# Optimization experiments

Hardware: AMD Instinct MI355X
Metric: run time of the kernel (lower is better)

Reference implementation:

```python
import jax, jax.numpy as jnp
import numpy as np

H = 16          # num_heads
HD = 64         # head_dim = latent_dim // num_heads
RHD = 32        # rope_head_dim = head_dim // 2
NHD = 32        # nope_head_dim
Q_LAT = 256     # latent_dim // compression_ratio
KV_LAT = 204    # xf_latent_dim // (compression_ratio + 1)
MAX_LEN = 2048
THETA = 10000.0
EPS = 1e-5


def _rope_tables():
    half = RHD // 2  # 16
    freqs = 1.0 / THETA ** (np.arange(half, dtype=np.float32) / half)
    t = np.arange(MAX_LEN, dtype=np.float32)
    ang = np.outer(t, freqs)  # (MAX_LEN, half)
    return jnp.asarray(np.cos(ang)), jnp.asarray(np.sin(ang))

COS, SIN = _rope_tables()


def _ln(x, g, b):
    m = jnp.mean(x, axis=-1, keepdims=True)
    v = jnp.var(x, axis=-1, keepdims=True)
    return (x - m) * jax.lax.rsqrt(v + EPS) * g + b


def _rope(t, cos, sin):
    # t: (..., L, RHD); cos/sin: (L, RHD//2); interleaved even/odd convention
    ev, od = t[..., 0::2], t[..., 1::2]
    oe = ev * cos - od * sin
    oo = ev * sin + od * cos
    return jnp.stack([oe, oo], axis=-1).reshape(t.shape)


def setup_inputs() -> dict:
    key = jax.random.key(0)
    ks = jax.random.split(key, 12)
    D = 1024
    s = 0.02
    return {
        "x": jax.random.normal(ks[0], (2, 2048, D), jnp.float32),
        "xf": jax.random.normal(ks[1], (2, 2048, D), jnp.float32),
        "Wqc": jax.random.normal(ks[2], (D, Q_LAT), jnp.float32) * s,
        "gq": jnp.ones((Q_LAT,), jnp.float32),
        "bq": jnp.zeros((Q_LAT,), jnp.float32),
        "Wq_rope": jax.random.normal(ks[3], (Q_LAT, H * RHD), jnp.float32) * s,
        "Wq_nope": jax.random.normal(ks[4], (Q_LAT, H * NHD), jnp.float32) * s,
        "Wkvc": jax.random.normal(ks[5], (D, KV_LAT), jnp.float32) * s,
        "gkv": jnp.ones((KV_LAT,), jnp.float32),
        "bkv": jnp.zeros((KV_LAT,), jnp.float32),
        "Wk_nope": jax.random.normal(ks[6], (KV_LAT, H * NHD), jnp.float32) * s,
        "Wv": jax.random.normal(ks[7], (KV_LAT, H * HD), jnp.float32) * s,
        "Wkr": jax.random.normal(ks[8], (D, RHD), jnp.float32) * s,
        "Wo": jax.random.normal(ks[9], (D, D), jnp.float32) * s,
        "bo": jnp.zeros((D,), jnp.float32),
    }


def reference(x, xf, Wqc, gq, bq, Wq_rope, Wq_nope, Wkvc, gkv, bkv, Wk_nope, Wv, Wkr, Wo, bo):
    B, T, D = x.shape
    S = xf.shape[1]

    # query path: compress -> LN -> decoupled decompress
    ql = _ln(x @ Wqc, gq, bq)                                   # (B,T,Q_LAT)
    q_nope = (ql @ Wq_nope).reshape(B, T, H, NHD).transpose(0, 2, 1, 3)  # (B,H,T,NHD)
    q_rope = (ql @ Wq_rope).reshape(B, T, H, RHD).transpose(0, 2, 1, 3)  # (B,H,T,RHD)

    # key/value path: compress -> LN -> decompress; shared single rope head
    kvl = _ln(xf @ Wkvc, gkv, bkv)                              # (B,S,KV_LAT)
    k_nope = (kvl @ Wk_nope).reshape(B, S, H, NHD).transpose(0, 2, 1, 3)  # (B,H,S,NHD)
    v = (kvl @ Wv).reshape(B, S, H, HD).transpose(0, 2, 1, 3)   # (B,H,S,HD)
    k_rope = (xf @ Wkr).reshape(B, S, 1, RHD).transpose(0, 2, 1, 3)       # (B,1,S,RHD)

    q_rope = _rope(q_rope, COS[:T], SIN[:T])
    k_rope = _rope(k_rope, COS[:S], SIN[:S]) / H
    k_rope = jnp.broadcast_to(k_rope, (B, H, S, RHD))

    q = jnp.concatenate([q_nope, q_rope], axis=-1)              # (B,H,T,HD)
    k = jnp.concatenate([k_nope, k_rope], axis=-1)              # (B,H,S,HD)

    scale = 1.0 / jnp.sqrt(jnp.asarray(HD, q.dtype))
    scores = jnp.einsum("bhtd,bhsd->bhts", q, k) * scale
    attn = jax.nn.softmax(scores, axis=-1)
    o = jnp.einsum("bhts,bhsd->bhtd", attn, v)                  # (B,H,T,HD)
    o = o.transpose(0, 2, 1, 3).reshape(B, T, H * HD)
    return o @ Wo + bo
```

## Files before the change

### kernel.cpp

```cpp
#include <hip/hip_runtime.h>
#include <hip/hip_bf16.h>
#include <math.h>

#define SEQ 2048

typedef __bf16 bf16x8 __attribute__((ext_vector_type(8)));
typedef float  f32x4  __attribute__((ext_vector_type(4)));

__device__ __forceinline__ unsigned short f2bf(float f) {
  __bf16 h = (__bf16)f;
  return __builtin_bit_cast(unsigned short, h);
}

__device__ __forceinline__ void gload16(const unsigned short* g, unsigned short* l) {
  __builtin_amdgcn_global_load_lds(
      (const __attribute__((address_space(1))) void*)g,
      (__attribute__((address_space(3))) void*)l, 16, 0, 0);
}

#define CLOG (0.125f * 1.44269504f)

struct WPrep {
  const float* src[8];
  unsigned short* dst[8];
  int K[8], N[8], NR[8], KC[8], nb[8];
  float2* cst;
};

__global__ __launch_bounds__(256) void wprep_kernel(WPrep p)
{
  __shared__ float tile[32][33];
  int bid = blockIdx.x;
  if (bid < 128) {
    const int idx = bid * 256 + threadIdx.x;
    const int pos = idx >> 4, i = idx & 15;
    const float freq = exp2f(-(float)i * 0.8304820237f);
    const float ang = (float)pos * freq;
    p.cst[idx] = make_float2(cosf(ang), sinf(ang));
    return;
  }
  bid -= 128;
  int di = 0;
  while (bid >= p.nb[di]) { bid -= p.nb[di]; ++di; }
  const float* src = p.src[di];
  unsigned short* dst = p.dst[di];
  const int K = p.K[di], N = p.N[di], KC = p.KC[di];
  const int nkx = KC >> 5;
  const int k0 = (bid % nkx) * 32, n0 = (bid / nkx) * 32;
  const int tx = threadIdx.x & 31, ty = threadIdx.x >> 5;
  for (int r = ty; r < 32; r += 8) {
    const int k = k0 + r, n = n0 + tx;
    tile[r][tx] = (k < K && n < N) ? src[(long)k * N + n] : 0.0f;
  }
  __syncthreads();
  for (int r = ty; r < 32; r += 8) {
    const int n = n0 + r, k = k0 + tx;
    dst[(long)n * KC + k] = f2bf(tile[tx][r]);
  }
}

template <int EPI, bool AF32>
__device__ __forceinline__ void gemm_body(
    unsigned short* smem,
    const void* __restrict__ Av, const unsigned short* __restrict__ BT,
    const float* __restrict__ bias, const float2* __restrict__ cst,
    void* __restrict__ C0v, void* __restrict__ C1v, int K, int N,
    int bx, int by)
{
  unsigned short* As = smem;
  unsigned short* Bs = smem + 2 * 128 * 32;
  const int tid = threadIdx.x;
  const int w = tid >> 6, lane = tid & 63;
  const int ln16 = lane & 15, quad = lane >> 4;
  const int wm = (w >> 1) * 64, wn = (w & 1) * 64;
  const int m0 = by * 128, n0 = bx * 128;
  const int rr = tid >> 2, cc = (tid & 3) * 8;

  const unsigned short* A = (const unsigned short*)Av;
  const float* Af = (const float*)Av;

  auto stageB = [&](int ib, int k0) {
    gload16(&BT[(long)(n0 + rr)      * K + k0 + cc], &Bs[ib * 4096 + rr * 32 + cc]);
    gload16(&BT[(long)(n0 + 64 + rr) * K + k0 + cc], &Bs[ib * 4096 + (64 + rr) * 32 + cc]);
  };
  auto stageAbf = [&](int ib, int k0) {
    gload16(&A[(long)(m0 + rr)      * K + k0 + cc], &As[ib * 4096 + rr * 32 + cc]);
    gload16(&A[(long)(m0 + 64 + rr) * K + k0 + cc], &As[ib * 4096 + (64 + rr) * 32 + cc]);
  };
  auto writeAf32 = [&](int ib, const float4& a0, const float4& a1,
                       const float4& a2, const float4& a3) {
    ushort4 u;
    u.x = f2bf(a0.x); u.y = f2bf(a0.y); u.z = f2bf(a0.z); u.w = f2bf(a0.w);
    *(ushort4*)&As[ib * 4096 + rr * 32 + cc] = u;
    u.x = f2bf(a1.x); u.y = f2bf(a1.y); u.z = f2bf(a1.z); u.w = f2bf(a1.w);
    *(ushort4*)&As[ib * 4096 + rr * 32 + cc + 4] = u;
    u.x = f2bf(a2.x); u.y = f2bf(a2.y); u.z = f2bf(a2.z); u.w = f2bf(a2.w);
    *(ushort4*)&As[ib * 4096 + (64 + rr) * 32 + cc] = u;
    u.x = f2bf(a3.x); u.y = f2bf(a3.y); u.z = f2bf(a3.z); u.w = f2bf(a3.w);
    *(ushort4*)&As[ib * 4096 + (64 + rr) * 32 + cc + 4] = u;
  };

  f32x4 acc[4][4];
#pragma unroll
  for (int i = 0; i < 4; ++i)
#pragma unroll
    for (int j = 0; j < 4; ++j)
#pragma unroll
      for (int r = 0; r < 4; ++r) acc[i][j][r] = 0.0f;

  stageB(0, 0);
  if (AF32) {
    float4 a0 = *(const float4*)&Af[(long)(m0 + rr)      * K + cc];
    float4 a1 = *(const float4*)&Af[(long)(m0 + rr)      * K + cc + 4];
    float4 a2 = *(const float4*)&Af[(long)(m0 + 64 + rr) * K + cc];
    float4 a3 = *(const float4*)&Af[(long)(m0 + 64 + rr) * K + cc + 4];
    writeAf32(0, a0, a1, a2, a3);
  } else {
    stageAbf(0, 0);
  }

  int ib = 0;
  for (int k0 = 0; k0 < K; k0 += 32, ib ^= 1) {
    __syncthreads();
    const int kn = k0 + 32;
    float4 a0, a1, a2, a3;
    if (kn < K) {
      stageB(ib ^ 1, kn);
      if (AF32) {
        a0 = *(const float4*)&Af[(long)(m0 + rr)      * K + kn + cc];
        a1 = *(const float4*)&Af[(long)(m0 + rr)      * K + kn + cc + 4];
        a2 = *(const float4*)&Af[(long)(m0 + 64 + rr) * K + kn + cc];
        a3 = *(const float4*)&Af[(long)(m0 + 64 + rr) * K + kn + cc + 4];
      } else {
        stageAbf(ib ^ 1, kn);
      }
    }
    bf16x8 fa[4], fb[4];
#pragma unroll
    for (int i = 0; i < 4; ++i) fa[i] = *(const bf16x8*)&As[ib * 4096 + (wm + i * 16 + ln16) * 32 + quad * 8];
#pragma unroll
    for (int j = 0; j < 4; ++j) fb[j] = *(const bf16x8*)&Bs[ib * 4096 + (wn + j * 16 + ln16) * 32 + quad * 8];
#pragma unroll
    for (int i = 0; i < 4; ++i)
#pragma unroll
      for (int j = 0; j < 4; ++j)
        acc[i][j] = __builtin_amdgcn_mfma_f32_16x16x32_bf16(fa[i], fb[j], acc[i][j], 0, 0, 0);
    if (AF32 && kn < K) writeAf32(ib ^ 1, a0, a1, a2, a3);
  }

#pragma unroll
  for (int i = 0; i < 4; ++i) {
    const int row0 = m0 + wm + i * 16 + quad * 4;
#pragma unroll
    for (int j = 0; j < 4; ++j) {
      const int col = n0 + wn + j * 16 + ln16;
      if (EPI == 0 || EPI == 1) {
        float* C = (float*)C0v;
        float bv = (EPI == 1) ? bias[col] : 0.0f;
#pragma unroll
        for (int r = 0; r < 4; ++r) C[(long)(row0 + r) * N + col] = acc[i][j][r] + bv;
      } else if (EPI == 3) {
        if (n0 < 512) {
          unsigned short* qn = (unsigned short*)C0v;
#pragma unroll
          for (int r = 0; r < 4; ++r) qn[(long)(row0 + r) * 512 + col] = f2bf(acc[i][j][r] * CLOG);
        } else {
          unsigned short* qr = (unsigned short*)C1v;
          const int c = col - 512;
          const int d = c & 31;
#pragma unroll
          for (int r = 0; r < 4; ++r) {
            const float v = acc[i][j][r];
            const float p = __shfl_xor(v, 1);
            const float2 t = cst[((row0 + r) & (SEQ - 1)) * 16 + (d >> 1)];
            const float o = ((d & 1) == 0) ? (v * t.x - p * t.y) : (p * t.y + v * t.x);
            qr[(long)(row0 + r) * 512 + c] = f2bf(o * CLOG);
          }
        }
      } else if (EPI == 4) {
        if (n0 < 256) {
          float* kvl = (float*)C0v;
#pragma unroll
          for (int r = 0; r < 4; ++r) kvl[(long)(row0 + r) * 256 + col] = acc[i][j][r];
        } else if (wn == 0 && j < 2) {
          unsigned short* kr = (unsigned short*)C1v;
          const int d = col - 256;
#pragma unroll
          for (int r = 0; r < 4; ++r) {
            const float v = acc[i][j][r];
            const float p = __shfl_xor(v, 1);
            const float2 t = cst[((row0 + r) & (SEQ - 1)) * 16 + (d >> 1)];
            const float o = ((d & 1) == 0) ? (v * t.x - p * t.y) : (p * t.y + v * t.x);
            kr[(long)(row0 + r) * 32 + d] = f2bf(o * 0.0625f);
          }
        }
      } else if (EPI == 5) {
        if (n0 < 512) {
          unsigned short* kn = (unsigned short*)C0v;
#pragma unroll
          for (int r = 0; r < 4; ++r) kn[(long)(row0 + r) * 512 + col] = f2bf(acc[i][j][r]);
        } else {
          unsigned short* vv = (unsigned short*)C1v;
          const int c = col - 512;
#pragma unroll
          for (int r = 0; r < 4; ++r) vv[(long)(row0 + r) * 1024 + c] = f2bf(acc[i][j][r]);
        }
      }
    }
  }
}

template <int EPI, bool AF32>
__global__ __launch_bounds__(256) void gemm_mfma(
    const void* __restrict__ Av, const unsigned short* __restrict__ BT,
    const float* __restrict__ bias, const float2* __restrict__ cst,
    void* __restrict__ C0v, void* __restrict__ C1v, int K, int N)
{
  __shared__ unsigned short smem[4 * 128 * 32];
  gemm_body<EPI, AF32>(smem, Av, BT, bias, cst, C0v, C1v, K, N, blockIdx.x, blockIdx.y);
}

template <int E0, bool AF0, int E1, bool AF1>
__global__ __launch_bounds__(256) void gemm_dual(
    const void* __restrict__ A0, const unsigned short* __restrict__ BT0,
    void* __restrict__ C00, void* __restrict__ C01, int K0, int N0, int nx0,
    const void* __restrict__ A1, const unsigned short* __restrict__ BT1,
    void* __restrict__ C10, void* __restrict__ C11, int K1, int N1,
    const float2* __restrict__ cst)
{
  __shared__ unsigned short smem[4 * 128 * 32];
  if (blockIdx.z == 0) {
    if ((int)blockIdx.x >= nx0) return;
    gemm_body<E0, AF0>(smem, A0, BT0, nullptr, cst, C00, C01, K0, N0, blockIdx.x, blockIdx.y);
  } else {
    gemm_body<E1, AF1>(smem, A1, BT1, nullptr, cst, C10, C11, K1, N1, blockIdx.x, blockIdx.y);
  }
}

__global__ __launch_bounds__(256) void ln2_kernel(
    const float* __restrict__ Xq, const float* __restrict__ Xkv,
    const float* __restrict__ gq, const float* __restrict__ bq,
    const float* __restrict__ gkv, const float* __restrict__ bkv,
    unsigned short* __restrict__ Yq, unsigned short* __restrict__ Ykv)
{
  const int row0 = blockIdx.x, tid = threadIdx.x;
  const bool isq = row0 < 4096;
  const int row = isq ? row0 : row0 - 4096;
  const float* X = isq ? Xq : Xkv;
  const float* g = isq ? gq : gkv;
  const float* b = isq ? bq : bkv;
  unsigned short* Y = isq ? Yq : Ykv;
  const int C = isq ? 256 : 204;
  const int Cp = isq ? 256 : 224;
  float v = (tid < C) ? X[(long)row * 256 + tid] : 0.0f;
  float s1 = v, s2 = v * v;
#pragma unroll
  for (int off = 1; off < 64; off <<= 1) {
    s1 += __shfl_xor(s1, off);
    s2 += __shfl_xor(s2, off);
  }
  __shared__ float rA[4], rB[4];
  const int wid = tid >> 6;
  if ((tid & 63) == 0) { rA[wid] = s1; rB[wid] = s2; }
  __syncthreads();
  s1 = rA[0] + rA[1] + rA[2] + rA[3];
  s2 = rB[0] + rB[1] + rB[2] + rB[3];
  const float mean = s1 / C;
  const float var  = s2 / C - mean * mean;
  const float r = rsqrtf(var + 1e-5f);
  if (tid < C) Y[(long)row * Cp + tid] = f2bf((v - mean) * r * g[tid] + b[tid]);
  else if (tid < Cp) Y[(long)row * Cp + tid] = 0;
}

__global__ __launch_bounds__(256) void transpose_v_kernel(
    const unsigned short* __restrict__ vf, unsigned short* __restrict__ vT)
{
  __shared__ unsigned short tile[64][72];
  const int bh = blockIdx.y;
  const int b = bh >> 4, h = bh & 15;
  const int s0 = blockIdx.x * 64;
  const int tid = threadIdx.x;
  for (int idx = tid; idx < 4096; idx += 256) {
    const int r = idx >> 6, c = idx & 63;
    tile[r][c] = vf[((long)b * SEQ + s0 + r) * 1024 + h * 64 + c];
  }
  __syncthreads();
  for (int idx = tid; idx < 4096; idx += 256) {
    const int d = idx >> 6, si = idx & 63;
    vT[((long)bh * 64 + d) * SEQ + s0 + si] = tile[si][d];
  }
}

#define KSTR 36
#define VSTR 68
#define PSTR 68
__global__ __launch_bounds__(256, 3) void attn_mfma_kernel(
    const unsigned short* __restrict__ qn, const unsigned short* __restrict__ qr,
    const unsigned short* __restrict__ kn, const unsigned short* __restrict__ kr,
    const unsigned short* __restrict__ vT, unsigned short* __restrict__ ob)
{
  __shared__ unsigned short Kn[2][64 * KSTR], Kr[2][64 * KSTR];
  __shared__ unsigned short Vs[2][64 * VSTR];
  __shared__ unsigned short Ps[128 * PSTR];
  const int bh = blockIdx.y;
  const int b = bh >> 4, h = bh & 15;
  const int t0 = blockIdx.x * 128;
  const int tid = threadIdx.x;
  const int w = tid >> 6, lane = tid & 63;
  const int ln16 = lane & 15, quad = lane >> 4;
  const int wrow = w * 32;
  const long bT = (long)b * SEQ;

  const int krow = tid >> 2, kc8 = (tid & 3) * 8;
  const int vd0 = tid >> 3, vc0 = (tid & 7) * 8;
  const int vd1 = (tid + 256) >> 3, vc1 = vc0;

  bf16x8 q0[2], q1[2];
#pragma unroll
  for (int g = 0; g < 2; ++g) {
    q0[g] = *(const bf16x8*)&qn[(bT + t0 + wrow + g * 16 + ln16) * 512 + h * 32 + quad * 8];
    q1[g] = *(const bf16x8*)&qr[(bT + t0 + wrow + g * 16 + ln16) * 512 + h * 32 + quad * 8];
  }

  auto loadKV = [&](int s0, bf16x8& rk0, bf16x8& rk1, bf16x8& rv0, bf16x8& rv1) {
    rk0 = *(const bf16x8*)&kn[(bT + s0 + krow) * 512 + h * 32 + kc8];
    rk1 = *(const bf16x8*)&kr[(bT + s0 + krow) * 32 + kc8];
    rv0 = *(const bf16x8*)&vT[((long)bh * 64 + vd0) * SEQ + s0 + vc0];
    rv1 = *(const bf16x8*)&vT[((long)bh * 64 + vd1) * SEQ + s0 + vc1];
  };
  auto writeKV = [&](int ib, bf16x8 rk0, bf16x8 rk1, bf16x8 rv0, bf16x8 rv1) {
    *(bf16x8*)&Kn[ib][krow * KSTR + kc8] = rk0;
    *(bf16x8*)&Kr[ib][krow * KSTR + kc8] = rk1;
    *(bf16x8*)&Vs[ib][vd0 * VSTR + vc0] = rv0;
    *(bf16x8*)&Vs[ib][vd1 * VSTR + vc1] = rv1;
  };

  bf16x8 ck0, ck1, cv0, cv1;
  bf16x8 nk0, nk1, nv0, nv1;
  loadKV(0, ck0, ck1, cv0, cv1);
  writeKV(0, ck0, ck1, cv0, cv1);
  loadKV(64, nk0, nk1, nv0, nv1);

  f32x4 o_acc[2][4];
#pragma unroll
  for (int g = 0; g < 2; ++g)
#pragma unroll
    for (int nt = 0; nt < 4; ++nt)
#pragma unroll
      for (int r = 0; r < 4; ++r) o_acc[g][nt][r] = 0.0f;
  float l_i[2] = {0.0f, 0.0f};

  int ib = 0;
  for (int s0 = 0; s0 < SEQ; s0 += 64, ib ^= 1) {
    __syncthreads();
    if (s0 + 64 < SEQ) {
      writeKV(ib ^ 1, nk0, nk1, nv0, nv1);
      if (s0 + 128 < SEQ) loadKV(s0 + 128, nk0, nk1, nv0, nv1);
    }

    bf16x8 kn_f[4], kr_f[4];
#pragma unroll
    for (int nt = 0; nt < 4; ++nt) {
      kn_f[nt] = *(const bf16x8*)&Kn[ib][(nt * 16 + ln16) * KSTR + quad * 8];
      kr_f[nt] = *(const bf16x8*)&Kr[ib][(nt * 16 + ln16) * KSTR + quad * 8];
    }

    f32x4 sf[2][4];
#pragma unroll
    for (int g = 0; g < 2; ++g) {
#pragma unroll
      for (int nt = 0; nt < 4; ++nt)
#pragma unroll
        for (int r = 0; r < 4; ++r) sf[g][nt][r] = 0.0f;
#pragma unroll
      for (int nt = 0; nt < 4; ++nt) {
        sf[g][nt] = __builtin_amdgcn_mfma_f32_16x16x32_bf16(kn_f[nt], q0[g], sf[g][nt], 0, 0, 0);
        sf[g][nt] = __builtin_amdgcn_mfma_f32_16x16x32_bf16(kr_f[nt], q1[g], sf[g][nt], 0, 0, 0);
      }
    }

#pragma unroll
    for (int g = 0; g < 2; ++g) {
      float rs = 0.0f;
      float pv[4][4];
#pragma unroll
      for (int nt = 0; nt < 4; ++nt)
#pragma unroll
        for (int r = 0; r < 4; ++r) {
          const float p = exp2f(sf[g][nt][r]);
          pv[nt][r] = p;
          rs += p;
        }
      rs += __shfl_xor(rs, 16);
      rs += __shfl_xor(rs, 32);
      l_i[g] += rs;
#pragma unroll
      for (int nt = 0; nt < 4; ++nt) {
        ushort4 u;
        u.x = f2bf(pv[nt][0]); u.y = f2bf(pv[nt][1]);
        u.z = f2bf(pv[nt][2]); u.w = f2bf(pv[nt][3]);
        *(ushort4*)&Ps[(wrow + g * 16 + ln16) * PSTR + nt * 16 + quad * 4] = u;
      }
    }

    bf16x8 v_f[2][4];
#pragma unroll
    for (int kk2 = 0; kk2 < 2; ++kk2)
#pragma unroll
      for (int nt = 0; nt < 4; ++nt)
        v_f[kk2][nt] = *(const bf16x8*)&Vs[ib][(nt * 16 + ln16) * VSTR + kk2 * 32 + quad * 8];

#pragma unroll
    for (int g = 0; g < 2; ++g) {
      bf16x8 a0 = *(const bf16x8*)&Ps[(wrow + g * 16 + ln16) * PSTR + quad * 8];
      bf16x8 a1 = *(const bf16x8*)&Ps[(wrow + g * 16 + ln16) * PSTR + 32 + quad * 8];
#pragma unroll
      for (int nt = 0; nt < 4; ++nt) {
        o_acc[g][nt] = __builtin_amdgcn_mfma_f32_16x16x32_bf16(a0, v_f[0][nt], o_acc[g][nt], 0, 0, 0);
        o_acc[g][nt] = __builtin_amdgcn_mfma_f32_16x16x32_bf16(a1, v_f[1][nt], o_acc[g][nt], 0, 0, 0);
      }
    }
  }

#pragma unroll
  for (int g = 0; g < 2; ++g) {
    const float lr = 1.0f / l_i[g];
    float lq[4];
#pragma unroll
    for (int r = 0; r < 4; ++r) lq[r] = __shfl(lr, quad * 4 + r);
#pragma unroll
    for (int r = 0; r < 4; ++r) {
      const long t = t0 + wrow + g * 16 + quad * 4 + r;
      const long base = (bT + t) * 1024 + h * 64 + ln16;
#pragma unroll
      for (int nt = 0; nt < 4; ++nt)
        ob[base + nt * 16] = f2bf(o_acc[g][nt][r] * lq[r]);
    }
  }
}

extern "C" void kernel_launch(void* const* d_in, const int* in_sizes, int n_in,
                              void* d_out, int out_size, void* d_ws, size_t ws_size,
                              hipStream_t stream) {
  const float* x       = (const float*)d_in[0];
  const float* xf      = (const float*)d_in[1];
  const float* Wqc     = (const float*)d_in[2];
  const float* gq      = (const float*)d_in[3];
  const float* bq      = (const float*)d_in[4];
  const float* Wq_rope = (const float*)d_in[5];
  const float* Wq_nope = (const float*)d_in[6];
  const float* Wkvc    = (const float*)d_in[7];
  const float* gkv     = (const float*)d_in[8];
  const float* bkv     = (const float*)d_in[9];
  const float* Wk_nope = (const float*)d_in[10];
  const float* Wv      = (const float*)d_in[11];
  const float* Wkr     = (const float*)d_in[12];
  const float* Wo      = (const float*)d_in[13];
  const float* bo      = (const float*)d_in[14];
  float* out = (float*)d_out;

  const long R = 4096;
  float* ws = (float*)d_ws;
  float* ql_f  = ws;
  float* kvl_f = ql_f + R * 256;
  float2* cst  = (float2*)(kvl_f + R * 256);
  unsigned short* us = (unsigned short*)(cst + 2048 * 16);
  unsigned short* ql_bf  = us;  us += R * 256;
  unsigned short* kvl_bf = us;  us += R * 224;
  unsigned short* qn_bf  = us;  us += R * 512;
  unsigned short* qr_bf  = us;  us += R * 512;
  unsigned short* kn_bf  = us;  us += R * 512;
  unsigned short* kr_bf  = us;  us += R * 32;
  unsigned short* v_bf   = us;  us += R * 1024;
  unsigned short* vT_bf  = us;  us += R * 1024;
  unsigned short* o_bf   = us;  us += R * 1024;
  unsigned short* WqcT   = us;  us += 256 * 1024;
  unsigned short* WkvkrT = us;  us += 384 * 1024;
  unsigned short* WqnqrT = us;  us += 1024 * 256;
  unsigned short* WknvT  = us;  us += 1536 * 224;
  unsigned short* WoT    = us;  us += 1024 * 1024;

  WPrep p;
  const float* srcs[8] = {Wqc, Wkvc, Wkr, Wq_nope, Wq_rope, Wk_nope, Wv, Wo};
  unsigned short* dsts[8] = {WqcT, WkvkrT, WkvkrT + 256 * 1024,
                             WqnqrT, WqnqrT + 512 * 256,
                             WknvT, WknvT + 512 * 224, WoT};
  const int Ks[8]  = {1024, 1024, 1024, 256, 256, 204, 204, 1024};
  const int Ns[8]  = {256, 204, 32, 512, 512, 512, 1024, 1024};
  const int NRs[8] = {256, 256, 128, 512, 512, 512, 1024, 1024};
  const int KCs[8] = {1024, 1024, 1024, 256, 256, 224, 224, 1024};
  int total = 128;
  for (int i = 0; i < 8; ++i) {
    p.src[i] = srcs[i]; p.dst[i] = dsts[i];
    p.K[i] = Ks[i]; p.N[i] = Ns[i]; p.NR[i] = NRs[i]; p.KC[i] = KCs[i];
    p.nb[i] = (KCs[i] / 32) * (NRs[i] / 32);
    total += p.nb[i];
  }
  p.cst = cst;
  wprep_kernel<<<total, 256, 0, stream>>>(p);

  gemm_dual<0, true, 4, true><<<dim3(3, 32, 2), 256, 0, stream>>>(
      x, WqcT, ql_f, nullptr, 1024, 256, 2,
      xf, WkvkrT, kvl_f, kr_bf, 1024, 384, cst);
  ln2_kernel<<<8192, 256, 0, stream>>>(ql_f, kvl_f, gq, bq, gkv, bkv, ql_bf, kvl_bf);
  gemm_dual<3, false, 5, false><<<dim3(12, 32, 2), 256, 0, stream>>>(
      ql_bf, WqnqrT, qn_bf, qr_bf, 256, 1024, 8,
      kvl_bf, WknvT, kn_bf, v_bf, 224, 1536, cst);
  transpose_v_kernel<<<dim3(32, 32), 256, 0, stream>>>(v_bf, vT_bf);
  attn_mfma_kernel<<<dim3(16, 32), 256, 0, stream>>>(qn_bf, qr_bf, kn_bf, kr_bf, vT_bf, o_bf);
  gemm_mfma<1, false><<<dim3(8, 32), 256, 0, stream>>>(o_bf, WoT, bo, nullptr, out, nullptr, 1024, 1024);
}
```

Measured before the change: 253.9 us.

## Fuse V transpose into GEMM epilogue and retile attention to 64-row blocks

The K/V decompression GEMM now stages its V output tile in shared memory and writes it directly in transposed (b,h,d,s) layout. This removes the separate transpose kernel and the intermediate v buffer. The attention kernel changes from 128 to 64 query rows per block (16 per wave), which doubles the grid to 1024 blocks and halves the P scratch. Block IDs are also remapped so each XCD handles a few heads, for L2 locality of K/V. The trade-off is that each K/V tile is now loaded twice as often, and the GEMM kernels need a larger shared-memory allocation.

```diff
diff --git a/kernel.cpp b/kernel.cpp
--- a/kernel.cpp
+++ b/kernel.cpp
@@ -148,6 +148,32 @@
     if (AF32 && kn < K) writeAf32(ib ^ 1, a0, a1, a2, a3);
   }
 
+  if (EPI == 5 && n0 >= 512) {
+    __syncthreads();
+#pragma unroll
+    for (int i = 0; i < 4; ++i) {
+      const int rl = wm + i * 16 + quad * 4;
+#pragma unroll
+      for (int j = 0; j < 4; ++j) {
+        const int cl = wn + j * 16 + ln16;
+        ushort4 u;
+        u.x = f2bf(acc[i][j][0]); u.y = f2bf(acc[i][j][1]);
+        u.z = f2bf(acc[i][j][2]); u.w = f2bf(acc[i][j][3]);
+        *(ushort4*)&smem[cl * 132 + rl] = u;
+      }
+    }
+    __syncthreads();
+    unsigned short* vT = (unsigned short*)C1v;
+    const int b = m0 >> 11, sbase = m0 & (SEQ - 1);
+    for (int q = tid; q < 128 * 16; q += 256) {
+      const int cl = q >> 4, sch = (q & 15) * 8;
+      bf16x8 val = *(const bf16x8*)&smem[cl * 132 + sch];
+      const int c = (n0 - 512) + cl;
+      const int hh = c >> 6, dd = c & 63;
+      *(bf16x8*)&vT[((long)(b * 16 + hh) * 64 + dd) * SEQ + sbase + sch] = val;
+    }
+    return;
+  }
 #pragma unroll
   for (int i = 0; i < 4; ++i) {
     const int row0 = m0 + wm + i * 16 + quad * 4;
@@ -195,16 +221,9 @@
           }
         }
       } else if (EPI == 5) {
-        if (n0 < 512) {
-          unsigned short* kn = (unsigned short*)C0v;
-#pragma unroll
-          for (int r = 0; r < 4; ++r) kn[(long)(row0 + r) * 512 + col] = f2bf(acc[i][j][r]);
-        } else {
-          unsigned short* vv = (unsigned short*)C1v;
-          const int c = col - 512;
-#pragma unroll
-          for (int r = 0; r < 4; ++r) vv[(long)(row0 + r) * 1024 + c] = f2bf(acc[i][j][r]);
-        }
+        unsigned short* kn = (unsigned short*)C0v;
+#pragma unroll
+        for (int r = 0; r < 4; ++r) kn[(long)(row0 + r) * 512 + col] = f2bf(acc[i][j][r]);
       }
     }
   }
@@ -216,7 +235,7 @@
     const float* __restrict__ bias, const float2* __restrict__ cst,
     void* __restrict__ C0v, void* __restrict__ C1v, int K, int N)
 {
-  __shared__ unsigned short smem[4 * 128 * 32];
+  __shared__ unsigned short smem[16896];
   gemm_body<EPI, AF32>(smem, Av, BT, bias, cst, C0v, C1v, K, N, blockIdx.x, blockIdx.y);
 }
 
@@ -228,7 +247,7 @@
     void* __restrict__ C10, void* __restrict__ C11, int K1, int N1,
     const float2* __restrict__ cst)
 {
-  __shared__ unsigned short smem[4 * 128 * 32];
+  __shared__ unsigned short smem[16896];
   if (blockIdx.z == 0) {
     if ((int)blockIdx.x >= nx0) return;
     gemm_body<E0, AF0>(smem, A0, BT0, nullptr, cst, C00, C01, K0, N0, blockIdx.x, blockIdx.y);
@@ -272,25 +291,6 @@
   else if (tid < Cp) Y[(long)row * Cp + tid] = 0;
 }
 
-__global__ __launch_bounds__(256) void transpose_v_kernel(
-    const unsigned short* __restrict__ vf, unsigned short* __restrict__ vT)
-{
-  __shared__ unsigned short tile[64][72];
-  const int bh = blockIdx.y;
-  const int b = bh >> 4, h = bh & 15;
-  const int s0 = blockIdx.x * 64;
-  const int tid = threadIdx.x;
-  for (int idx = tid; idx < 4096; idx += 256) {
-    const int r = idx >> 6, c = idx & 63;
-    tile[r][c] = vf[((long)b * SEQ + s0 + r) * 1024 + h * 64 + c];
-  }
-  __syncthreads();
-  for (int idx = tid; idx < 4096; idx += 256) {
-    const int d = idx >> 6, si = idx & 63;
-    vT[((long)bh * 64 + d) * SEQ + s0 + si] = tile[si][d];
-  }
-}
-
 #define KSTR 36
 #define VSTR 68
 #define PSTR 68
@@ -301,38 +301,37 @@
 {
   __shared__ unsigned short Kn[2][64 * KSTR], Kr[2][64 * KSTR];
   __shared__ unsigned short Vs[2][64 * VSTR];
-  __shared__ unsigned short Ps[128 * PSTR];
-  const int bh = blockIdx.y;
+  __shared__ unsigned short Ps[64 * PSTR];
+  const int id = blockIdx.x;
+  const int xcd = id & 7, j = id >> 3;
+  const int bh = xcd * 4 + (j & 3);
+  const int tile = j >> 2;
   const int b = bh >> 4, h = bh & 15;
-  const int t0 = blockIdx.x * 128;
+  const int t0 = tile * 64;
   const int tid = threadIdx.x;
   const int w = tid >> 6, lane = tid & 63;
   const int ln16 = lane & 15, quad = lane >> 4;
-  const int wrow = w * 32;
+  const int trow = w * 16;
   const long bT = (long)b * SEQ;
 
   const int krow = tid >> 2, kc8 = (tid & 3) * 8;
   const int vd0 = tid >> 3, vc0 = (tid & 7) * 8;
-  const int vd1 = (tid + 256) >> 3, vc1 = vc0;
-
-  bf16x8 q0[2], q1[2];
-#pragma unroll
-  for (int g = 0; g < 2; ++g) {
-    q0[g] = *(const bf16x8*)&qn[(bT + t0 + wrow + g * 16 + ln16) * 512 + h * 32 + quad * 8];
-    q1[g] = *(const bf16x8*)&qr[(bT + t0 + wrow + g * 16 + ln16) * 512 + h * 32 + quad * 8];
-  }
+  const int vd1 = vd0 + 32;
+
+  bf16x8 q0 = *(const bf16x8*)&qn[(bT + t0 + trow + ln16) * 512 + h * 32 + quad * 8];
+  bf16x8 q1 = *(const bf16x8*)&qr[(bT + t0 + trow + ln16) * 512 + h * 32 + quad * 8];
 
   auto loadKV = [&](int s0, bf16x8& rk0, bf16x8& rk1, bf16x8& rv0, bf16x8& rv1) {
     rk0 = *(const bf16x8*)&kn[(bT + s0 + krow) * 512 + h * 32 + kc8];
     rk1 = *(const bf16x8*)&kr[(bT + s0 + krow) * 32 + kc8];
     rv0 = *(const bf16x8*)&vT[((long)bh * 64 + vd0) * SEQ + s0 + vc0];
-    rv1 = *(const bf16x8*)&vT[((long)bh * 64 + vd1) * SEQ + s0 + vc1];
+    rv1 = *(const bf16x8*)&vT[((long)bh * 64 + vd1) * SEQ + s0 + vc0];
   };
   auto writeKV = [&](int ib, bf16x8 rk0, bf16x8 rk1, bf16x8 rv0, bf16x8 rv1) {
     *(bf16x8*)&Kn[ib][krow * KSTR + kc8] = rk0;
     *(bf16x8*)&Kr[ib][krow * KSTR + kc8] = rk1;
     *(bf16x8*)&Vs[ib][vd0 * VSTR + vc0] = rv0;
-    *(bf16x8*)&Vs[ib][vd1 * VSTR + vc1] = rv1;
+    *(bf16x8*)&Vs[ib][vd1 * VSTR + vc0] = rv1;
   };
 
   bf16x8 ck0, ck1, cv0, cv1;
@@ -341,14 +340,12 @@
   writeKV(0, ck0, ck1, cv0, cv1);
   loadKV(64, nk0, nk1, nv0, nv1);
 
-  f32x4 o_acc[2][4];
-#pragma unroll
-  for (int g = 0; g < 2; ++g)
-#pragma unroll
-    for (int nt = 0; nt < 4; ++nt)
-#pragma unroll
-      for (int r = 0; r < 4; ++r) o_acc[g][nt][r] = 0.0f;
-  float l_i[2] = {0.0f, 0.0f};
+  f32x4 o_acc[4];
+#pragma unroll
+  for (int nt = 0; nt < 4; ++nt)
+#pragma unroll
+    for (int r = 0; r < 4; ++r) o_acc[nt][r] = 0.0f;
+  float l_i = 0.0f;
 
   int ib = 0;
   for (int s0 = 0; s0 < SEQ; s0 += 64, ib ^= 1) {
@@ -358,84 +355,62 @@
       if (s0 + 128 < SEQ) loadKV(s0 + 128, nk0, nk1, nv0, nv1);
     }
 
-    bf16x8 kn_f[4], kr_f[4];
+    f32x4 sf[4];
+#pragma unroll
+    for (int nt = 0; nt < 4; ++nt)
+#pragma unroll
+      for (int r = 0; r < 4; ++r) sf[nt][r] = 0.0f;
 #pragma unroll
     for (int nt = 0; nt < 4; ++nt) {
-      kn_f[nt] = *(const bf16x8*)&Kn[ib][(nt * 16 + ln16) * KSTR + quad * 8];
-      kr_f[nt] = *(const bf16x8*)&Kr[ib][(nt * 16 + ln16) * KSTR + quad * 8];
-    }
-
-    f32x4 sf[2][4];
-#pragma unroll
-    for (int g = 0; g < 2; ++g) {
-#pragma unroll
-      for (int nt = 0; nt < 4; ++nt)
-#pragma unroll
-        for (int r = 0; r < 4; ++r) sf[g][nt][r] = 0.0f;
-#pragma unroll
-      for (int nt = 0; nt < 4; ++nt) {
-        sf[g][nt] = __builtin_amdgcn_mfma_f32_16x16x32_bf16(kn_f[nt], q0[g], sf[g][nt], 0, 0, 0);
-        sf[g][nt] = __builtin_amdgcn_mfma_f32_16x16x32_bf16(kr_f[nt], q1[g], sf[g][nt], 0, 0, 0);
+      bf16x8 a0 = *(const bf16x8*)&Kn[ib][(nt * 16 + ln16) * KSTR + quad * 8];
+      sf[nt] = __builtin_amdgcn_mfma_f32_16x16x32_bf16(a0, q0, sf[nt], 0, 0, 0);
+      bf16x8 a1 = *(const bf16x8*)&Kr[ib][(nt * 16 + ln16) * KSTR + quad * 8];
+      sf[nt] = __builtin_amdgcn_mfma_f32_16x16x32_bf16(a1, q1, sf[nt], 0, 0, 0);
+    }
+
+    float rs = 0.0f;
+    float pv[4][4];
+#pragma unroll
+    for (int nt = 0; nt < 4; ++nt)
+#pragma unroll
+      for (int r = 0; r < 4; ++r) {
+        const float p = exp2f(sf[nt][r]);
+        pv[nt][r] = p;
+        rs += p;
       }
-    }
-
-#pragma unroll
-    for (int g = 0; g < 2; ++g) {
-      float rs = 0.0f;
-      float pv[4][4];
-#pragma unroll
-      for (int nt = 0; nt < 4; ++nt)
-#pragma unroll
-        for (int r = 0; r < 4; ++r) {
-          const float p = exp2f(sf[g][nt][r]);
-          pv[nt][r] = p;
-          rs += p;
-        }
-      rs += __shfl_xor(rs, 16);
-      rs += __shfl_xor(rs, 32);
-      l_i[g] += rs;
-#pragma unroll
-      for (int nt = 0; nt < 4; ++nt) {
-        ushort4 u;
-        u.x = f2bf(pv[nt][0]); u.y = f2bf(pv[nt][1]);
-        u.z = f2bf(pv[nt][2]); u.w = f2bf(pv[nt][3]);
-        *(ushort4*)&Ps[(wrow + g * 16 + ln16) * PSTR + nt * 16 + quad * 4] = u;
-      }
-    }
-
-    bf16x8 v_f[2][4];
-#pragma unroll
-    for (int kk2 = 0; kk2 < 2; ++kk2)
-#pragma unroll
-      for (int nt = 0; nt < 4; ++nt)
-        v_f[kk2][nt] = *(const bf16x8*)&Vs[ib][(nt * 16 + ln16) * VSTR + kk2 * 32 + quad * 8];
-
-#pragma unroll
-    for (int g = 0; g < 2; ++g) {
-      bf16x8 a0 = *(const bf16x8*)&Ps[(wrow + g * 16 + ln16) * PSTR + quad * 8];
-      bf16x8 a1 = *(const bf16x8*)&Ps[(wrow + g * 16 + ln16) * PSTR + 32 + quad * 8];
-#pragma unroll
-      for (int nt = 0; nt < 4; ++nt) {
-        o_acc[g][nt] = __builtin_amdgcn_mfma_f32_16x16x32_bf16(a0, v_f[0][nt], o_acc[g][nt], 0, 0, 0);
-        o_acc[g][nt] = __builtin_amdgcn_mfma_f32_16x16x32_bf16(a1, v_f[1][nt], o_acc[g][nt], 0, 0, 0);
-      }
-    }
-  }
-
-#pragma unroll
-  for (int g = 0; g < 2; ++g) {
-    const float lr = 1.0f / l_i[g];
-    float lq[4];
-#pragma unroll
-    for (int r = 0; r < 4; ++r) lq[r] = __shfl(lr, quad * 4 + r);
-#pragma unroll
-    for (int r = 0; r < 4; ++r) {
-      const long t = t0 + wrow + g * 16 + quad * 4 + r;
-      const long base = (bT + t) * 1024 + h * 64 + ln16;
-#pragma unroll
-      for (int nt = 0; nt < 4; ++nt)
-        ob[base + nt * 16] = f2bf(o_acc[g][nt][r] * lq[r]);
-    }
+    rs += __shfl_xor(rs, 16);
+    rs += __shfl_xor(rs, 32);
+    l_i += rs;
+#pragma unroll
+    for (int nt = 0; nt < 4; ++nt) {
+      ushort4 u;
+      u.x = f2bf(pv[nt][0]); u.y = f2bf(pv[nt][1]);
+      u.z = f2bf(pv[nt][2]); u.w = f2bf(pv[nt][3]);
+      *(ushort4*)&Ps[(trow + ln16) * PSTR + nt * 16 + quad * 4] = u;
+    }
+
+    bf16x8 a0 = *(const bf16x8*)&Ps[(trow + ln16) * PSTR + quad * 8];
+    bf16x8 a1 = *(const bf16x8*)&Ps[(trow + ln16) * PSTR + 32 + quad * 8];
+#pragma unroll
+    for (int nt = 0; nt < 4; ++nt) {
+      bf16x8 v0 = *(const bf16x8*)&Vs[ib][(nt * 16 + ln16) * VSTR + quad * 8];
+      o_acc[nt] = __builtin_amdgcn_mfma_f32_16x16x32_bf16(a0, v0, o_acc[nt], 0, 0, 0);
+      bf16x8 v1 = *(const bf16x8*)&Vs[ib][(nt * 16 + ln16) * VSTR + 32 + quad * 8];
+      o_acc[nt] = __builtin_amdgcn_mfma_f32_16x16x32_bf16(a1, v1, o_acc[nt], 0, 0, 0);
+    }
+  }
+
+  const float lr = 1.0f / l_i;
+  float lq[4];
+#pragma unroll
+  for (int r = 0; r < 4; ++r) lq[r] = __shfl(lr, quad * 4 + r);
+#pragma unroll
+  for (int r = 0; r < 4; ++r) {
+    const long t = t0 + trow + quad * 4 + r;
+    const long base = (bT + t) * 1024 + h * 64 + ln16;
+#pragma unroll
+    for (int nt = 0; nt < 4; ++nt)
+      ob[base + nt * 16] = f2bf(o_acc[nt][r] * lq[r]);
   }
 }
 
@@ -471,7 +446,6 @@
   unsigned short* qr_bf  = us;  us += R * 512;
   unsigned short* kn_bf  = us;  us += R * 512;
   unsigned short* kr_bf  = us;  us += R * 32;
-  unsigned short* v_bf   = us;  us += R * 1024;
   unsigned short* vT_bf  = us;  us += R * 1024;
   unsigned short* o_bf   = us;  us += R * 1024;
   unsigned short* WqcT   = us;  us += 256 * 1024;
@@ -505,8 +479,7 @@
   ln2_kernel<<<8192, 256, 0, stream>>>(ql_f, kvl_f, gq, bq, gkv, bkv, ql_bf, kvl_bf);
   gemm_dual<3, false, 5, false><<<dim3(12, 32, 2), 256, 0, stream>>>(
       ql_bf, WqnqrT, qn_bf, qr_bf, 256, 1024, 8,
-      kvl_bf, WknvT, kn_bf, v_bf, 224, 1536, cst);
-  transpose_v_kernel<<<dim3(32, 32), 256, 0, stream>>>(v_bf, vT_bf);
-  attn_mfma_kernel<<<dim3(16, 32), 256, 0, stream>>>(qn_bf, qr_bf, kn_bf, kr_bf, vT_bf, o_bf);
+      kvl_bf, WknvT, kn_bf, vT_bf, 224, 1536, cst);
+  attn_mfma_kernel<<<1024, 256, 0, stream>>>(qn_bf, qr_bf, kn_bf, kr_bf, vT_bf, o_bf);
   gemm_mfma<1, false><<<dim3(8, 32), 256, 0, stream>>>(o_bf, WoT, bo, nullptr, out, nullptr, 1024, 1024);
 }
```

Result: slower. 260.3 us (+2.5%).
